# Kernel tuning notes

Measured on AMD Instinct MI355X. Metric: run time of the kernel, lower is better.

## Reference

```python
import jax, jax.numpy as jnp
import numpy as np

N, E, IN_CH, HID, EDGE_DIM, L, G = 50000, 800000, 64, 128, 16, 3, 256

def _bn(h, g, b):
    # BatchNorm1d in training mode (biased batch variance), eps=1e-5
    m = h.mean(0)
    v = ((h - m) ** 2).mean(0)
    return (h - m) * jax.lax.rsqrt(v + 1e-5) * g + b

def setup_inputs() -> dict:
    key = jax.random.key(0)
    ks = jax.random.split(key, 24)
    s = 0.05
    inp = {
        'x': jax.random.normal(ks[0], (N, IN_CH), jnp.float32),
        'edge_attr': jax.random.uniform(ks[1], (E, EDGE_DIM), jnp.float32),
        'src': jax.random.randint(ks[2], (E,), 0, N, jnp.int32),
        'dst': jax.random.randint(ks[3], (E,), 0, N, jnp.int32),
        'batch': jnp.sort(jax.random.randint(ks[4], (N,), 0, G, jnp.int32)),
        'Wp': jax.random.normal(ks[5], (IN_CH, HID), jnp.float32) * s,
        'bp': jnp.zeros((HID,), jnp.float32),
        'conv_We': jax.random.normal(ks[6], (L, EDGE_DIM, HID), jnp.float32) * s,
        'conv_be': jnp.zeros((L, HID), jnp.float32),
        'conv_W1': jax.random.normal(ks[7], (L, HID, HID), jnp.float32) * s,
        'conv_b1': jnp.zeros((L, HID), jnp.float32),
        'conv_g1': jnp.ones((L, HID), jnp.float32),
        'conv_bt1': jnp.zeros((L, HID), jnp.float32),
        'conv_W2': jax.random.normal(ks[8], (L, HID, HID), jnp.float32) * s,
        'conv_b2': jnp.zeros((L, HID), jnp.float32),
        'bn_g': jnp.ones((L, HID), jnp.float32),
        'bn_b': jnp.zeros((L, HID), jnp.float32),
        'head_W1': jax.random.normal(ks[9], (HID * L * 2, HID), jnp.float32) * s,
        'head_b1': jnp.zeros((HID,), jnp.float32),
        'head_g': jnp.ones((HID,), jnp.float32),
        'head_bt': jnp.zeros((HID,), jnp.float32),
        'head_W2': jax.random.normal(ks[10], (HID, 1), jnp.float32) * s,
        'head_b2': jnp.zeros((1,), jnp.float32),
    }
    return inp

def reference(x, edge_attr, src, dst, batch, Wp, bp, conv_We, conv_be, conv_W1, conv_b1,
              conv_g1, conv_bt1, conv_W2, conv_b2, bn_g, bn_b, head_W1, head_b1,
              head_g, head_bt, head_W2, head_b2):
    n = x.shape[0]
    h = x @ Wp + bp  # [N, HID]
    outs = []
    for l in range(L):
        # GINEConv: msg = ReLU(x_src + lin(edge_attr)); sum-aggregate to dst; (1+eps)*x + agg, eps=0
        ee = edge_attr @ conv_We[l] + conv_be[l]          # [E, HID]
        msg = jax.nn.relu(h[src] + ee)                     # [E, HID]
        agg = jax.ops.segment_sum(msg, dst, num_segments=n)
        t = h + agg
        t = t @ conv_W1[l] + conv_b1[l]
        t = jax.nn.relu(_bn(t, conv_g1[l], conv_bt1[l]))
        t = t @ conv_W2[l] + conv_b2[l]
        h = jax.nn.relu(_bn(t, bn_g[l], bn_b[l]))          # outer BN + ReLU (dropout = identity, eval)
        outs.append(h)
    xj = jnp.concatenate(outs, axis=-1)                    # JK 'cat' -> [N, 3*HID]
    cnt = jax.ops.segment_sum(jnp.ones((n,), xj.dtype), batch, num_segments=G)
    z_mean = jax.ops.segment_sum(xj, batch, num_segments=G) / jnp.clip(cnt, 1.0)[:, None]
    z_max = jax.ops.segment_max(xj, batch, num_segments=G)
    z = jnp.concatenate([z_mean, z_max], axis=-1)          # [G, 6*HID]
    z = z @ head_W1 + head_b1
    z = jax.nn.relu(_bn(z, head_g, head_bt))
    return (z @ head_W2 + head_b2).squeeze(-1)             # [G]
```

## Files before the change

kernel.cpp:

```cpp
#include <hip/hip_runtime.h>
#include <hip/hip_bf16.h>

#define HID 128
#define EDIM 16

typedef float v4f __attribute__((ext_vector_type(4)));
typedef float v2f __attribute__((ext_vector_type(2)));
typedef short s8v __attribute__((ext_vector_type(8)));
typedef float f4v __attribute__((ext_vector_type(4)));

#define MFMA_BF16(a, b, c) __builtin_amdgcn_mfma_f32_16x16x32_bf16((a), (b), (c), 0, 0, 0)

__device__ __forceinline__ unsigned short bf16_rne(float v)
{
    unsigned u = __builtin_bit_cast(unsigned, v);
    return (unsigned short)((u + 0x7fffu + ((u >> 16) & 1u)) >> 16);
}

__device__ __forceinline__ void split_bf16(float v, unsigned short& h, unsigned short& l)
{
    unsigned u = __builtin_bit_cast(unsigned, v);
    unsigned hu = (u + 0x7fffu + ((u >> 16) & 1u)) >> 16;
    h = (unsigned short)hu;
    float hf = __builtin_bit_cast(float, hu << 16);
    l = bf16_rne(v - hf);
}

__device__ __forceinline__ v2f vmax0(v2f a)
{
    v2f r; r.x = fmaxf(a.x, 0.f); r.y = fmaxf(a.y, 0.f); return r;
}

__global__ void hist_kernel(const int* __restrict__ dst, int* __restrict__ deg, int E)
{
    int e = blockIdx.x * 256 + threadIdx.x;
    if (e < E) atomicAdd(&deg[dst[e]], 1);
}

__global__ void block_sum_kernel(const int* __restrict__ deg, int* __restrict__ bsum, int Nn)
{
    int i = blockIdx.x * 256 + threadIdx.x;
    int v = (i < Nn) ? deg[i] : 0;
#pragma unroll
    for (int off = 32; off > 0; off >>= 1) v += __shfl_down(v, off, 64);
    __shared__ int ws[4];
    if ((threadIdx.x & 63) == 0) ws[threadIdx.x >> 6] = v;
    __syncthreads();
    if (threadIdx.x == 0) bsum[blockIdx.x] = ws[0] + ws[1] + ws[2] + ws[3];
}

__global__ void bsum_scan_kernel(int* bsum, int nb, int* total_out)
{
    __shared__ int sh[256];
    int tid = threadIdx.x;
    int v = (tid < nb) ? bsum[tid] : 0;
    sh[tid] = v;
    __syncthreads();
    for (int off = 1; off < 256; off <<= 1) {
        int tv = (tid >= off) ? sh[tid - off] : 0;
        __syncthreads();
        sh[tid] += tv;
        __syncthreads();
    }
    if (tid < nb) bsum[tid] = sh[tid] - v;
    if (tid == 255) *total_out = sh[255];
}

__global__ void block_scan_kernel(const int* __restrict__ deg, const int* __restrict__ bsum,
                                  int* __restrict__ row_start, int* __restrict__ cursor, int Nn)
{
    __shared__ int sh[256];
    int tid = threadIdx.x;
    int i = blockIdx.x * 256 + tid;
    int v = (i < Nn) ? deg[i] : 0;
    sh[tid] = v;
    __syncthreads();
    for (int off = 1; off < 256; off <<= 1) {
        int tv = (tid >= off) ? sh[tid - off] : 0;
        __syncthreads();
        sh[tid] += tv;
        __syncthreads();
    }
    if (i < Nn) {
        int excl = sh[tid] - v + bsum[blockIdx.x];
        row_start[i] = excl;
        cursor[i] = excl;
    }
}

template<bool COPY_EA>
__global__ void scatter_kernel(const int* __restrict__ src, const int* __restrict__ dst,
                               int* cursor, int* __restrict__ perm,
                               int* __restrict__ src_perm,
                               const float* __restrict__ ea, float* __restrict__ ea_perm,
                               int E)
{
    int e = blockIdx.x * 256 + threadIdx.x;
    if (e >= E) return;
    int pos = atomicAdd(&cursor[dst[e]], 1);
    src_perm[pos] = src[e];
    if (COPY_EA) {
        const float4* s4 = (const float4*)(ea + (size_t)e * EDIM);
        float4* d4 = (float4*)(ea_perm + (size_t)pos * EDIM);
        d4[0] = s4[0]; d4[1] = s4[1]; d4[2] = s4[2]; d4[3] = s4[3];
    } else {
        perm[pos] = e;
    }
}

__global__ void prep_weights(const float* __restrict__ Wp, const float* __restrict__ W1,
                             const float* __restrict__ W2, unsigned short* __restrict__ out)
{
    int idx = blockIdx.x * 256 + threadIdx.x;
    if (idx < 8192) {
        int n = idx >> 6, k = idx & 63;
        unsigned short h, l;
        split_bf16(Wp[k * 128 + n], h, l);
        out[idx] = h;
        out[8192 + idx] = l;
    } else {
        int j = idx - 8192;
        if (j >= 6 * 16384) return;
        int m2 = j >> 14;
        int r = j & 16383;
        int n = r >> 7, k = r & 127;
        int l = m2 >> 1;
        const float* Wsrc = (m2 & 1) ? (W2 + l * 16384) : (W1 + l * 16384);
        unsigned short h, lo;
        split_bf16(Wsrc[k * 128 + n], h, lo);
        int base = 16384 + m2 * 32768;
        out[base + r] = h;
        out[base + 16384 + r] = lo;
    }
}

__device__ __forceinline__ void matvp(const v4f& a0, const v4f& a1,
                                      const v4f& a2, const v4f& a3,
                                      const v2f* __restrict__ w, v2f& m)
{
    m += w[0] * a0.x;  m += w[1] * a0.y;  m += w[2] * a0.z;  m += w[3] * a0.w;
    m += w[4] * a1.x;  m += w[5] * a1.y;  m += w[6] * a1.z;  m += w[7] * a1.w;
    m += w[8] * a2.x;  m += w[9] * a2.y;  m += w[10] * a2.z; m += w[11] * a2.w;
    m += w[12] * a3.x; m += w[13] * a3.y; m += w[14] * a3.z; m += w[15] * a3.w;
}

template<bool GATH>
__global__ __launch_bounds__(256, 6) void aggregate_kernel(
    const float* __restrict__ h, const float* __restrict__ eaG,
    const int* __restrict__ perm, const int* __restrict__ src_perm,
    const int* __restrict__ row_start,
    const float* __restrict__ We, const float* __restrict__ be,
    float* __restrict__ t, int Nn)
{
    int tid = threadIdx.x;
    int c = (tid & 63) * 2;
    v2f w[16];
#pragma unroll
    for (int k = 0; k < 16; ++k) w[k] = *(const v2f*)&We[k * HID + c];
    v2f bj = *(const v2f*)&be[c];
    int node = blockIdx.x * 4 + (tid >> 6);
    if (node >= Nn) return;
    const float* __restrict__ hc = h + c;
    v2f acc = *(const v2f*)(hc + ((unsigned)node << 7));
    int p0 = __builtin_amdgcn_readfirstlane(row_start[node]);
    int p1 = __builtin_amdgcn_readfirstlane(row_start[node + 1]);
    int p = p0;
    int s0 = 0, s1 = 0, s2 = 0, s3 = 0;
    if (p + 4 <= p1) { s0 = src_perm[p]; s1 = src_perm[p + 1]; s2 = src_perm[p + 2]; s3 = src_perm[p + 3]; }
    while (p + 4 <= p1) {
        int np = p + 4;
        int t0 = 0, t1 = 0, t2 = 0, t3 = 0;
        if (np + 4 <= p1) { t0 = src_perm[np]; t1 = src_perm[np + 1]; t2 = src_perm[np + 2]; t3 = src_perm[np + 3]; }
        v2f h0 = *(const v2f*)(hc + ((unsigned)s0 << 7));
        v2f h1 = *(const v2f*)(hc + ((unsigned)s1 << 7));
        v2f h2 = *(const v2f*)(hc + ((unsigned)s2 << 7));
        v2f h3 = *(const v2f*)(hc + ((unsigned)s3 << 7));
        int q0, q1, q2, q3;
        if (GATH) { q0 = p; q1 = p + 1; q2 = p + 2; q3 = p + 3; }
        else      { q0 = perm[p]; q1 = perm[p + 1]; q2 = perm[p + 2]; q3 = perm[p + 3]; }
        const v4f* e0 = (const v4f*)(eaG + (size_t)(unsigned)q0 * EDIM);
        const v4f* e1 = (const v4f*)(eaG + (size_t)(unsigned)q1 * EDIM);
        const v4f* e2 = (const v4f*)(eaG + (size_t)(unsigned)q2 * EDIM);
        const v4f* e3 = (const v4f*)(eaG + (size_t)(unsigned)q3 * EDIM);
        v4f a00 = e0[0], a01 = e0[1], a02 = e0[2], a03 = e0[3];
        v4f a10 = e1[0], a11 = e1[1], a12 = e1[2], a13 = e1[3];
        v4f a20 = e2[0], a21 = e2[1], a22 = e2[2], a23 = e2[3];
        v4f a30 = e3[0], a31 = e3[1], a32 = e3[2], a33 = e3[3];
        v2f m0 = bj + h0, m1 = bj + h1, m2 = bj + h2, m3 = bj + h3;
        matvp(a00, a01, a02, a03, w, m0);
        matvp(a10, a11, a12, a13, w, m1);
        matvp(a20, a21, a22, a23, w, m2);
        matvp(a30, a31, a32, a33, w, m3);
        acc += vmax0(m0) + vmax0(m1) + vmax0(m2) + vmax0(m3);
        p = np;
        s0 = t0; s1 = t1; s2 = t2; s3 = t3;
    }
    for (; p < p1; ++p) {
        int s = src_perm[p];
        int q = GATH ? p : perm[p];
        const v4f* e0 = (const v4f*)(eaG + (size_t)(unsigned)q * EDIM);
        v4f a0 = e0[0], a1 = e0[1], a2 = e0[2], a3 = e0[3];
        v2f hv = *(const v2f*)(hc + ((unsigned)s << 7));
        v2f m0 = bj + hv;
        matvp(a0, a1, a2, a3, w, m0);
        acc += vmax0(m0);
    }
    *(v2f*)(t + ((unsigned)node << 7) + c) = acc;
}

#define LPAD 40

template<int K, bool PRE_BN, bool POST_STATS>
__global__ __launch_bounds__(256) void gemm_mfma(
    const float* __restrict__ A, const unsigned short* __restrict__ Wh,
    const unsigned short* __restrict__ Wl, const float* __restrict__ bias,
    const float* __restrict__ preStats, const float* __restrict__ preG, const float* __restrict__ preB,
    float* __restrict__ C, float* __restrict__ postStats, int Nrows, float invN)
{
    __shared__ __align__(16) unsigned short Ah[128 * LPAD], Al[128 * LPAD];
    __shared__ __align__(16) unsigned short Bh[128 * LPAD], Bl[128 * LPAD];
    __shared__ float sc[PRE_BN ? K : 1], sb[PRE_BN ? K : 1];
    int tid = threadIdx.x;
    int rbase = blockIdx.x * 128;
    if (PRE_BN) {
        if (tid < K) {
            float mean = preStats[tid] * invN;
            float var = preStats[K + tid] * invN - mean * mean;
            float rstd = rsqrtf(var + 1e-5f);
            float g = preG[tid];
            sc[tid] = rstd * g;
            sb[tid] = preB[tid] - mean * rstd * g;
        }
        __syncthreads();
    }
    int w = tid >> 6, nl = tid & 15, q = (tid >> 4) & 3;
    f4v acc[2][8];
#pragma unroll
    for (int mt = 0; mt < 2; ++mt)
#pragma unroll
        for (int nt = 0; nt < 8; ++nt)
#pragma unroll
            for (int r = 0; r < 4; ++r) acc[mt][nt][r] = 0.f;

    for (int ks = 0; ks < K / 32; ++ks) {
        int k0 = ks * 32;
        if (ks) __syncthreads();
#pragma unroll
        for (int i = 0; i < 4; ++i) {
            int cidx = tid + i * 256;
            int m = cidx >> 3, k4 = (cidx & 7) * 4;
            int gr = rbase + m;
            float4 v = make_float4(0.f, 0.f, 0.f, 0.f);
            if (gr < Nrows) v = *(const float4*)&A[(size_t)gr * K + k0 + k4];
            if (PRE_BN) {
                v.x = fmaxf(v.x * sc[k0 + k4]     + sb[k0 + k4],     0.f);
                v.y = fmaxf(v.y * sc[k0 + k4 + 1] + sb[k0 + k4 + 1], 0.f);
                v.z = fmaxf(v.z * sc[k0 + k4 + 2] + sb[k0 + k4 + 2], 0.f);
                v.w = fmaxf(v.w * sc[k0 + k4 + 3] + sb[k0 + k4 + 3], 0.f);
            }
            unsigned short h0, l0, h1, l1, h2, l2, h3, l3;
            split_bf16(v.x, h0, l0); split_bf16(v.y, h1, l1);
            split_bf16(v.z, h2, l2); split_bf16(v.w, h3, l3);
            uint2 hp, lp;
            hp.x = (unsigned)h0 | ((unsigned)h1 << 16); hp.y = (unsigned)h2 | ((unsigned)h3 << 16);
            lp.x = (unsigned)l0 | ((unsigned)l1 << 16); lp.y = (unsigned)l2 | ((unsigned)l3 << 16);
            *(uint2*)&Ah[m * LPAD + k4] = hp;
            *(uint2*)&Al[m * LPAD + k4] = lp;
        }
#pragma unroll
        for (int i = 0; i < 2; ++i) {
            int g = tid + i * 256;
            int n = g >> 2, kq = (g & 3) * 8;
            uint4 hv = *(const uint4*)&Wh[(size_t)n * K + k0 + kq];
            uint4 lv = *(const uint4*)&Wl[(size_t)n * K + k0 + kq];
            *(uint4*)&Bh[n * LPAD + kq] = hv;
            *(uint4*)&Bl[n * LPAD + kq] = lv;
        }
        __syncthreads();
        s8v ah0 = *(const s8v*)&Ah[(w * 32 + nl) * LPAD + q * 8];
        s8v ah1 = *(const s8v*)&Ah[(w * 32 + 16 + nl) * LPAD + q * 8];
        s8v al0 = *(const s8v*)&Al[(w * 32 + nl) * LPAD + q * 8];
        s8v al1 = *(const s8v*)&Al[(w * 32 + 16 + nl) * LPAD + q * 8];
#pragma unroll
        for (int nt = 0; nt < 8; ++nt) {
            s8v bh = *(const s8v*)&Bh[(nt * 16 + nl) * LPAD + q * 8];
            s8v bl = *(const s8v*)&Bl[(nt * 16 + nl) * LPAD + q * 8];
            acc[0][nt] = MFMA_BF16(ah0, bh, acc[0][nt]);
            acc[0][nt] = MFMA_BF16(ah0, bl, acc[0][nt]);
            acc[0][nt] = MFMA_BF16(al0, bh, acc[0][nt]);
            acc[1][nt] = MFMA_BF16(ah1, bh, acc[1][nt]);
            acc[1][nt] = MFMA_BF16(ah1, bl, acc[1][nt]);
            acc[1][nt] = MFMA_BF16(al1, bh, acc[1][nt]);
        }
    }
    __syncthreads();

    float* redS = (float*)Ah;
    float* redQ = (float*)Al;
#pragma unroll
    for (int nt = 0; nt < 8; ++nt) {
        int col = nt * 16 + nl;
        float bcol = bias[col];
        float sv = 0.f, qv = 0.f;
#pragma unroll
        for (int mt = 0; mt < 2; ++mt) {
#pragma unroll
            for (int r = 0; r < 4; ++r) {
                int grow = rbase + w * 32 + mt * 16 + q * 4 + r;
                if (grow < Nrows) {
                    float o = acc[mt][nt][r] + bcol;
                    C[(size_t)grow * HID + col] = o;
                    if (POST_STATS) { sv += o; qv += o * o; }
                }
            }
        }
        if (POST_STATS) {
            sv += __shfl_down(sv, 32, 64); sv += __shfl_down(sv, 16, 64);
            qv += __shfl_down(qv, 32, 64); qv += __shfl_down(qv, 16, 64);
            if ((tid & 63) < 16) { redS[w * 128 + col] = sv; redQ[w * 128 + col] = qv; }
        }
    }
    if (POST_STATS) {
        __syncthreads();
        if (tid < 128) {
            float S = redS[tid] + redS[128 + tid] + redS[256 + tid] + redS[384 + tid];
            float Q = redQ[tid] + redQ[128 + tid] + redQ[256 + tid] + redQ[384 + tid];
            atomicAdd(&postStats[tid], S);
            atomicAdd(&postStats[128 + tid], Q);
        }
    }
}

__global__ void bn_apply_pool(const float* __restrict__ X, float* __restrict__ h,
                              const float* __restrict__ stats, const float* __restrict__ g,
                              const float* __restrict__ b, const int* __restrict__ starts,
                              float* __restrict__ z, int l, float invN)
{
    int gph = blockIdx.x;
    int tid = threadIdx.x;
    int ch4 = (tid & 31) * 4, wk = tid >> 5;
    float sc[4], sh[4];
#pragma unroll
    for (int u = 0; u < 4; ++u) {
        int j = ch4 + u;
        float mean = stats[j] * invN;
        float var = stats[128 + j] * invN - mean * mean;
        float rstd = rsqrtf(var + 1e-5f);
        float gg = g[j];
        sc[u] = rstd * gg;
        sh[u] = b[j] - mean * rstd * gg;
    }
    int s = starts[gph], e = starts[gph + 1];
    float4 sum = make_float4(0.f, 0.f, 0.f, 0.f);
    float4 mx = make_float4(0.f, 0.f, 0.f, 0.f);
    for (int n = s + wk; n < e; n += 16) {
        float4 v = *(const float4*)&X[(size_t)n * HID + ch4];
        v.x = fmaxf(v.x * sc[0] + sh[0], 0.f);
        v.y = fmaxf(v.y * sc[1] + sh[1], 0.f);
        v.z = fmaxf(v.z * sc[2] + sh[2], 0.f);
        v.w = fmaxf(v.w * sc[3] + sh[3], 0.f);
        *(float4*)&h[(size_t)n * HID + ch4] = v;
        sum.x += v.x; sum.y += v.y; sum.z += v.z; sum.w += v.w;
        mx.x = fmaxf(mx.x, v.x); mx.y = fmaxf(mx.y, v.y);
        mx.z = fmaxf(mx.z, v.z); mx.w = fmaxf(mx.w, v.w);
    }
    __shared__ float ls[16 * 128], lm[16 * 128];
    *(float4*)&ls[wk * 128 + ch4] = sum;
    *(float4*)&lm[wk * 128 + ch4] = mx;
    __syncthreads();
    if (tid < 128) {
        float S = 0.f, M = 0.f;
#pragma unroll
        for (int k = 0; k < 16; ++k) {
            S += ls[k * 128 + tid];
            M = fmaxf(M, lm[k * 128 + tid]);
        }
        float cnt = (float)(e - s);
        z[(size_t)gph * 768 + l * 128 + tid] = S / fmaxf(cnt, 1.f);
        z[(size_t)gph * 768 + 384 + l * 128 + tid] = M;
    }
}

__global__ void starts_kernel(const int* __restrict__ batch, int* __restrict__ starts,
                              int Nn, int Gn)
{
    int g = blockIdx.x * blockDim.x + threadIdx.x;
    if (g > Gn) return;
    int lo = 0, hi = Nn;
    while (lo < hi) { int mid = (lo + hi) >> 1; if (batch[mid] < g) lo = mid + 1; else hi = mid; }
    starts[g] = lo;
}

__global__ void head_gemm1(const float* __restrict__ z, const float* __restrict__ W,
                           const float* __restrict__ bias, float* __restrict__ zr,
                           float* __restrict__ msums)
{
    __shared__ __align__(16) float zl[768];
    int g = blockIdx.x, j = threadIdx.x;
    for (int i = j; i < 768; i += 128) zl[i] = z[(size_t)g * 768 + i];
    __syncthreads();
    float acc = bias[j];
    for (int k = 0; k < 768; k += 4) {
        float4 a4 = *(const float4*)&zl[k];
        acc += a4.x * W[k * 128 + j] + a4.y * W[(k + 1) * 128 + j]
             + a4.z * W[(k + 2) * 128 + j] + a4.w * W[(k + 3) * 128 + j];
    }
    zr[(size_t)g * 128 + j] = acc;
    atomicAdd(&msums[j], acc);
    atomicAdd(&msums[128 + j], acc * acc);
}

__global__ void head_final(const float* __restrict__ zr, const float* __restrict__ msums,
                           const float* __restrict__ hg, const float* __restrict__ hb,
                           const float* __restrict__ W2, const float* __restrict__ b2,
                           float* __restrict__ out, float invG)
{
    int g = blockIdx.x, j = threadIdx.x;
    float mean = msums[j] * invG;
    float var = msums[128 + j] * invG - mean * mean;
    float rstd = rsqrtf(var + 1e-5f);
    float v = zr[(size_t)g * 128 + j];
    v = (v - mean) * rstd * hg[j] + hb[j];
    v = fmaxf(v, 0.f);
    float p = v * W2[j];
#pragma unroll
    for (int off = 32; off > 0; off >>= 1) p += __shfl_down(p, off, 64);
    __shared__ float partial[2];
    if ((j & 63) == 0) partial[j >> 6] = p;
    __syncthreads();
    if (j == 0) out[g] = partial[0] + partial[1] + b2[0];
}

extern "C" void kernel_launch(void* const* d_in, const int* in_sizes, int n_in,
                              void* d_out, int out_size, void* d_ws, size_t ws_size,
                              hipStream_t stream)
{
    const float* x         = (const float*)d_in[0];
    const float* edge_attr = (const float*)d_in[1];
    const int*   src       = (const int*)d_in[2];
    const int*   dst       = (const int*)d_in[3];
    const int*   batch     = (const int*)d_in[4];
    const float* Wp        = (const float*)d_in[5];
    const float* bp        = (const float*)d_in[6];
    const float* conv_We   = (const float*)d_in[7];
    const float* conv_be   = (const float*)d_in[8];
    const float* conv_W1   = (const float*)d_in[9];
    const float* conv_b1   = (const float*)d_in[10];
    const float* conv_g1   = (const float*)d_in[11];
    const float* conv_bt1  = (const float*)d_in[12];
    const float* conv_W2   = (const float*)d_in[13];
    const float* conv_b2   = (const float*)d_in[14];
    const float* bn_g      = (const float*)d_in[15];
    const float* bn_b      = (const float*)d_in[16];
    const float* head_W1   = (const float*)d_in[17];
    const float* head_b1   = (const float*)d_in[18];
    const float* head_g    = (const float*)d_in[19];
    const float* head_bt   = (const float*)d_in[20];
    const float* head_W2   = (const float*)d_in[21];
    const float* head_b2   = (const float*)d_in[22];

    const int N = in_sizes[4];
    const int E = in_sizes[2];
    const int G = out_size;
    const int L = 3;

    float* h        = (float*)d_ws;
    float* t        = h + (size_t)N * HID;
    float* z        = t + (size_t)N * HID;
    float* zr       = z + (size_t)G * 768;
    float* statsAll = zr + (size_t)G * HID;
    int*   deg      = (int*)(statsAll + 7 * 256);
    int*   starts   = deg + N;
    int*   row_start= starts + (G + 1);
    int*   cursor   = row_start + (N + 1);
    int*   bsum     = cursor + N;
    int*   src_perm = bsum + 256;
    int*   perm     = src_perm + E;
    unsigned short* wt = (unsigned short*)(perm + E);
    size_t base_end = (size_t)((char*)(wt + 212992) - (char*)d_ws);
    size_t ea_off = (base_end + 15) & ~(size_t)15;
    bool gath = (ea_off + (size_t)E * EDIM * sizeof(float)) <= ws_size;
    float* ea_perm = (float*)((char*)d_ws + ea_off);
    float* msums = statsAll + 6 * 256;

    (void)n_in;

    const float invN = 1.0f / (float)N;
    const float invG = 1.0f / (float)G;
    const int nb = (N + 255) / 256;
    const int gemmBlocks = (N + 127) / 128;

    (void)hipMemsetAsync(statsAll, 0, 7 * 256 * sizeof(float) + (size_t)N * sizeof(int), stream);
    hist_kernel<<<(E + 255) / 256, 256, 0, stream>>>(dst, deg, E);
    block_sum_kernel<<<nb, 256, 0, stream>>>(deg, bsum, N);
    bsum_scan_kernel<<<1, 256, 0, stream>>>(bsum, nb, &row_start[N]);
    block_scan_kernel<<<nb, 256, 0, stream>>>(deg, bsum, row_start, cursor, N);
    if (gath)
        scatter_kernel<true><<<(E + 255) / 256, 256, 0, stream>>>(
            src, dst, cursor, perm, src_perm, edge_attr, ea_perm, E);
    else
        scatter_kernel<false><<<(E + 255) / 256, 256, 0, stream>>>(
            src, dst, cursor, perm, src_perm, edge_attr, ea_perm, E);
    starts_kernel<<<1, 512, 0, stream>>>(batch, starts, N, G);
    prep_weights<<<(8192 + 6 * 16384 + 255) / 256, 256, 0, stream>>>(Wp, conv_W1, conv_W2, wt);

    const unsigned short* Wp_hi = wt;
    const unsigned short* Wp_lo = wt + 8192;

    gemm_mfma<64, false, false><<<gemmBlocks, 256, 0, stream>>>(
        x, Wp_hi, Wp_lo, bp, nullptr, nullptr, nullptr, h, nullptr, N, invN);

    for (int l = 0; l < L; ++l) {
        float* sI = statsAll + l * 512;
        float* sO = sI + 256;
        const unsigned short* W1hi = wt + 16384 + (size_t)(2 * l) * 32768;
        const unsigned short* W1lo = W1hi + 16384;
        const unsigned short* W2hi = wt + 16384 + (size_t)(2 * l + 1) * 32768;
        const unsigned short* W2lo = W2hi + 16384;
        if (gath)
            aggregate_kernel<true><<<(N + 3) / 4, 256, 0, stream>>>(
                h, ea_perm, perm, src_perm, row_start,
                conv_We + (size_t)l * EDIM * HID, conv_be + l * HID, t, N);
        else
            aggregate_kernel<false><<<(N + 3) / 4, 256, 0, stream>>>(
                h, edge_attr, perm, src_perm, row_start,
                conv_We + (size_t)l * EDIM * HID, conv_be + l * HID, t, N);
        gemm_mfma<128, false, true><<<gemmBlocks, 256, 0, stream>>>(
            t, W1hi, W1lo, conv_b1 + l * HID,
            nullptr, nullptr, nullptr, t, sI, N, invN);
        gemm_mfma<128, true, true><<<gemmBlocks, 256, 0, stream>>>(
            t, W2hi, W2lo, conv_b2 + l * HID,
            sI, conv_g1 + l * HID, conv_bt1 + l * HID, t, sO, N, invN);
        bn_apply_pool<<<G, 512, 0, stream>>>(
            t, h, sO, bn_g + l * HID, bn_b + l * HID, starts, z, l, invN);
    }

    head_gemm1<<<G, 128, 0, stream>>>(z, head_W1, head_b1, zr, msums);
    head_final<<<G, 128, 0, stream>>>(zr, msums, head_g, head_bt, head_W2, head_b2,
                                      (float*)d_out, invG);
}
```

Measured before the change: 719.2 us.

## Store node features and permuted edge attributes as bf16 to halve gather traffic

Node features h and the dst-sorted edge attributes are now stored in bf16 instead of fp32. The projection GEMM and the BN/pool kernel write packed bf16, and the aggregation kernel unpacks these values on load. This targets the memory-bound gathers in aggregation and also raises the occupancy hint. Non-temporal stores are used in the scatter kernel. The cost is reduced precision on h and edge_attr, which may affect accuracy against the fp32 reference.

```diff
diff --git a/kernel.cpp b/kernel.cpp
--- a/kernel.cpp
+++ b/kernel.cpp
@@ -6,6 +6,7 @@
 
 typedef float v4f __attribute__((ext_vector_type(4)));
 typedef float v2f __attribute__((ext_vector_type(2)));
+typedef unsigned v4u __attribute__((ext_vector_type(4)));
 typedef short s8v __attribute__((ext_vector_type(8)));
 typedef float f4v __attribute__((ext_vector_type(4)));
 
@@ -15,6 +16,24 @@
 {
     unsigned u = __builtin_bit_cast(unsigned, v);
     return (unsigned short)((u + 0x7fffu + ((u >> 16) & 1u)) >> 16);
+}
+
+__device__ __forceinline__ unsigned pack2(float lo, float hi)
+{
+    return (unsigned)bf16_rne(lo) | ((unsigned)bf16_rne(hi) << 16);
+}
+
+__device__ __forceinline__ float bflo(unsigned u) { return __builtin_bit_cast(float, u << 16); }
+__device__ __forceinline__ float bfhi(unsigned u) { return __builtin_bit_cast(float, u & 0xffff0000u); }
+
+__device__ __forceinline__ v2f unpack2(unsigned u)
+{
+    v2f r; r.x = bflo(u); r.y = bfhi(u); return r;
+}
+
+__device__ __forceinline__ v4f unpack4(unsigned a, unsigned b)
+{
+    v4f r; r.x = bflo(a); r.y = bfhi(a); r.z = bflo(b); r.w = bfhi(b); return r;
 }
 
 __device__ __forceinline__ void split_bf16(float v, unsigned short& h, unsigned short& l)
@@ -92,17 +111,24 @@
 __global__ void scatter_kernel(const int* __restrict__ src, const int* __restrict__ dst,
                                int* cursor, int* __restrict__ perm,
                                int* __restrict__ src_perm,
-                               const float* __restrict__ ea, float* __restrict__ ea_perm,
+                               const float* __restrict__ ea, unsigned short* __restrict__ ea16,
                                int E)
 {
     int e = blockIdx.x * 256 + threadIdx.x;
     if (e >= E) return;
     int pos = atomicAdd(&cursor[dst[e]], 1);
-    src_perm[pos] = src[e];
+    __builtin_nontemporal_store(src[e], &src_perm[pos]);
     if (COPY_EA) {
         const float4* s4 = (const float4*)(ea + (size_t)e * EDIM);
-        float4* d4 = (float4*)(ea_perm + (size_t)pos * EDIM);
-        d4[0] = s4[0]; d4[1] = s4[1]; d4[2] = s4[2]; d4[3] = s4[3];
+        float4 a = s4[0], b = s4[1], c = s4[2], d = s4[3];
+        v4u u0, u1;
+        u0.x = pack2(a.x, a.y); u0.y = pack2(a.z, a.w);
+        u0.z = pack2(b.x, b.y); u0.w = pack2(b.z, b.w);
+        u1.x = pack2(c.x, c.y); u1.y = pack2(c.z, c.w);
+        u1.z = pack2(d.x, d.y); u1.w = pack2(d.z, d.w);
+        v4u* dp = (v4u*)(ea16 + (size_t)pos * EDIM);
+        __builtin_nontemporal_store(u0, dp);
+        __builtin_nontemporal_store(u1, dp + 1);
     } else {
         perm[pos] = e;
     }
@@ -145,63 +171,86 @@
 }
 
 template<bool GATH>
-__global__ __launch_bounds__(256, 6) void aggregate_kernel(
-    const float* __restrict__ h, const float* __restrict__ eaG,
+__global__ __launch_bounds__(256, 8) void aggregate_kernel(
+    const unsigned short* __restrict__ h16, const unsigned short* __restrict__ ea16,
+    const float* __restrict__ eaf,
     const int* __restrict__ perm, const int* __restrict__ src_perm,
     const int* __restrict__ row_start,
     const float* __restrict__ We, const float* __restrict__ be,
     float* __restrict__ t, int Nn)
 {
     int tid = threadIdx.x;
-    int c = (tid & 63) * 2;
+    int lane = tid & 63;
+    int c = lane * 2;
     v2f w[16];
 #pragma unroll
     for (int k = 0; k < 16; ++k) w[k] = *(const v2f*)&We[k * HID + c];
     v2f bj = *(const v2f*)&be[c];
     int node = blockIdx.x * 4 + (tid >> 6);
     if (node >= Nn) return;
-    const float* __restrict__ hc = h + c;
-    v2f acc = *(const v2f*)(hc + ((unsigned)node << 7));
+    const unsigned* __restrict__ hw = (const unsigned*)h16 + lane;
+    v2f acc = unpack2(hw[(unsigned)node << 6]);
     int p0 = __builtin_amdgcn_readfirstlane(row_start[node]);
     int p1 = __builtin_amdgcn_readfirstlane(row_start[node + 1]);
     int p = p0;
+    const unsigned* ep = (const unsigned*)ea16 + (size_t)(unsigned)p0 * 8u;
     int s0 = 0, s1 = 0, s2 = 0, s3 = 0;
     if (p + 4 <= p1) { s0 = src_perm[p]; s1 = src_perm[p + 1]; s2 = src_perm[p + 2]; s3 = src_perm[p + 3]; }
     while (p + 4 <= p1) {
         int np = p + 4;
         int t0 = 0, t1 = 0, t2 = 0, t3 = 0;
         if (np + 4 <= p1) { t0 = src_perm[np]; t1 = src_perm[np + 1]; t2 = src_perm[np + 2]; t3 = src_perm[np + 3]; }
-        v2f h0 = *(const v2f*)(hc + ((unsigned)s0 << 7));
-        v2f h1 = *(const v2f*)(hc + ((unsigned)s1 << 7));
-        v2f h2 = *(const v2f*)(hc + ((unsigned)s2 << 7));
-        v2f h3 = *(const v2f*)(hc + ((unsigned)s3 << 7));
-        int q0, q1, q2, q3;
-        if (GATH) { q0 = p; q1 = p + 1; q2 = p + 2; q3 = p + 3; }
-        else      { q0 = perm[p]; q1 = perm[p + 1]; q2 = perm[p + 2]; q3 = perm[p + 3]; }
-        const v4f* e0 = (const v4f*)(eaG + (size_t)(unsigned)q0 * EDIM);
-        const v4f* e1 = (const v4f*)(eaG + (size_t)(unsigned)q1 * EDIM);
-        const v4f* e2 = (const v4f*)(eaG + (size_t)(unsigned)q2 * EDIM);
-        const v4f* e3 = (const v4f*)(eaG + (size_t)(unsigned)q3 * EDIM);
-        v4f a00 = e0[0], a01 = e0[1], a02 = e0[2], a03 = e0[3];
-        v4f a10 = e1[0], a11 = e1[1], a12 = e1[2], a13 = e1[3];
-        v4f a20 = e2[0], a21 = e2[1], a22 = e2[2], a23 = e2[3];
-        v4f a30 = e3[0], a31 = e3[1], a32 = e3[2], a33 = e3[3];
-        v2f m0 = bj + h0, m1 = bj + h1, m2 = bj + h2, m3 = bj + h3;
+        unsigned hu0 = hw[(unsigned)s0 << 6];
+        unsigned hu1 = hw[(unsigned)s1 << 6];
+        unsigned hu2 = hw[(unsigned)s2 << 6];
+        unsigned hu3 = hw[(unsigned)s3 << 6];
+        v4f a00, a01, a02, a03, a10, a11, a12, a13;
+        v4f a20, a21, a22, a23, a30, a31, a32, a33;
+        if (GATH) {
+            unsigned ua[32];
+#pragma unroll
+            for (int i = 0; i < 32; ++i) ua[i] = ep[i];
+            a00 = unpack4(ua[0], ua[1]);   a01 = unpack4(ua[2], ua[3]);
+            a02 = unpack4(ua[4], ua[5]);   a03 = unpack4(ua[6], ua[7]);
+            a10 = unpack4(ua[8], ua[9]);   a11 = unpack4(ua[10], ua[11]);
+            a12 = unpack4(ua[12], ua[13]); a13 = unpack4(ua[14], ua[15]);
+            a20 = unpack4(ua[16], ua[17]); a21 = unpack4(ua[18], ua[19]);
+            a22 = unpack4(ua[20], ua[21]); a23 = unpack4(ua[22], ua[23]);
+            a30 = unpack4(ua[24], ua[25]); a31 = unpack4(ua[26], ua[27]);
+            a32 = unpack4(ua[28], ua[29]); a33 = unpack4(ua[30], ua[31]);
+        } else {
+            const v4f* e0 = (const v4f*)(eaf + (size_t)(unsigned)perm[p] * EDIM);
+            const v4f* e1 = (const v4f*)(eaf + (size_t)(unsigned)perm[p + 1] * EDIM);
+            const v4f* e2 = (const v4f*)(eaf + (size_t)(unsigned)perm[p + 2] * EDIM);
+            const v4f* e3 = (const v4f*)(eaf + (size_t)(unsigned)perm[p + 3] * EDIM);
+            a00 = e0[0]; a01 = e0[1]; a02 = e0[2]; a03 = e0[3];
+            a10 = e1[0]; a11 = e1[1]; a12 = e1[2]; a13 = e1[3];
+            a20 = e2[0]; a21 = e2[1]; a22 = e2[2]; a23 = e2[3];
+            a30 = e3[0]; a31 = e3[1]; a32 = e3[2]; a33 = e3[3];
+        }
+        v2f m0 = bj + unpack2(hu0), m1 = bj + unpack2(hu1);
+        v2f m2 = bj + unpack2(hu2), m3 = bj + unpack2(hu3);
         matvp(a00, a01, a02, a03, w, m0);
         matvp(a10, a11, a12, a13, w, m1);
         matvp(a20, a21, a22, a23, w, m2);
         matvp(a30, a31, a32, a33, w, m3);
         acc += vmax0(m0) + vmax0(m1) + vmax0(m2) + vmax0(m3);
+        ep += 32;
         p = np;
         s0 = t0; s1 = t1; s2 = t2; s3 = t3;
     }
     for (; p < p1; ++p) {
         int s = src_perm[p];
-        int q = GATH ? p : perm[p];
-        const v4f* e0 = (const v4f*)(eaG + (size_t)(unsigned)q * EDIM);
-        v4f a0 = e0[0], a1 = e0[1], a2 = e0[2], a3 = e0[3];
-        v2f hv = *(const v2f*)(hc + ((unsigned)s << 7));
-        v2f m0 = bj + hv;
+        v4f a0, a1, a2, a3;
+        if (GATH) {
+            const unsigned* er = (const unsigned*)ea16 + (size_t)(unsigned)p * 8u;
+            a0 = unpack4(er[0], er[1]); a1 = unpack4(er[2], er[3]);
+            a2 = unpack4(er[4], er[5]); a3 = unpack4(er[6], er[7]);
+        } else {
+            const v4f* e0 = (const v4f*)(eaf + (size_t)(unsigned)perm[p] * EDIM);
+            a0 = e0[0]; a1 = e0[1]; a2 = e0[2]; a3 = e0[3];
+        }
+        v2f m0 = bj + unpack2(hw[(unsigned)s << 6]);
         matvp(a0, a1, a2, a3, w, m0);
         acc += vmax0(m0);
     }
@@ -210,12 +259,12 @@
 
 #define LPAD 40
 
-template<int K, bool PRE_BN, bool POST_STATS>
+template<int K, bool PRE_BN, bool POST_STATS, bool OUT_BF16>
 __global__ __launch_bounds__(256) void gemm_mfma(
     const float* __restrict__ A, const unsigned short* __restrict__ Wh,
     const unsigned short* __restrict__ Wl, const float* __restrict__ bias,
     const float* __restrict__ preStats, const float* __restrict__ preG, const float* __restrict__ preB,
-    float* __restrict__ C, float* __restrict__ postStats, int Nrows, float invN)
+    void* __restrict__ Cout, float* __restrict__ postStats, int Nrows, float invN)
 {
     __shared__ __align__(16) unsigned short Ah[128 * LPAD], Al[128 * LPAD];
     __shared__ __align__(16) unsigned short Bh[128 * LPAD], Bl[128 * LPAD];
@@ -295,6 +344,8 @@
     }
     __syncthreads();
 
+    float* Cf = (float*)Cout;
+    unsigned short* Ch = (unsigned short*)Cout;
     float* redS = (float*)Ah;
     float* redQ = (float*)Al;
 #pragma unroll
@@ -309,7 +360,8 @@
                 int grow = rbase + w * 32 + mt * 16 + q * 4 + r;
                 if (grow < Nrows) {
                     float o = acc[mt][nt][r] + bcol;
-                    C[(size_t)grow * HID + col] = o;
+                    if (OUT_BF16) Ch[(size_t)grow * HID + col] = bf16_rne(o);
+                    else          Cf[(size_t)grow * HID + col] = o;
                     if (POST_STATS) { sv += o; qv += o * o; }
                 }
             }
@@ -331,7 +383,7 @@
     }
 }
 
-__global__ void bn_apply_pool(const float* __restrict__ X, float* __restrict__ h,
+__global__ void bn_apply_pool(const float* __restrict__ X, unsigned short* __restrict__ h16,
                               const float* __restrict__ stats, const float* __restrict__ g,
                               const float* __restrict__ b, const int* __restrict__ starts,
                               float* __restrict__ z, int l, float invN)
@@ -353,13 +405,17 @@
     int s = starts[gph], e = starts[gph + 1];
     float4 sum = make_float4(0.f, 0.f, 0.f, 0.f);
     float4 mx = make_float4(0.f, 0.f, 0.f, 0.f);
+    unsigned* hv32 = (unsigned*)h16;
     for (int n = s + wk; n < e; n += 16) {
         float4 v = *(const float4*)&X[(size_t)n * HID + ch4];
         v.x = fmaxf(v.x * sc[0] + sh[0], 0.f);
         v.y = fmaxf(v.y * sc[1] + sh[1], 0.f);
         v.z = fmaxf(v.z * sc[2] + sh[2], 0.f);
         v.w = fmaxf(v.w * sc[3] + sh[3], 0.f);
-        *(float4*)&h[(size_t)n * HID + ch4] = v;
+        uint2 pk;
+        pk.x = pack2(v.x, v.y);
+        pk.y = pack2(v.z, v.w);
+        *(uint2*)&hv32[(size_t)n * 64 + (ch4 >> 1)] = pk;
         sum.x += v.x; sum.y += v.y; sum.z += v.z; sum.w += v.w;
         mx.x = fmaxf(mx.x, v.x); mx.y = fmaxf(mx.y, v.y);
         mx.z = fmaxf(mx.z, v.z); mx.w = fmaxf(mx.w, v.w);
@@ -464,9 +520,9 @@
     const int G = out_size;
     const int L = 3;
 
-    float* h        = (float*)d_ws;
-    float* t        = h + (size_t)N * HID;
-    float* z        = t + (size_t)N * HID;
+    float* t        = (float*)d_ws;
+    unsigned short* h16 = (unsigned short*)(t + (size_t)N * HID);
+    float* z        = (float*)(h16 + (size_t)N * HID);
     float* zr       = z + (size_t)G * 768;
     float* statsAll = zr + (size_t)G * HID;
     int*   deg      = (int*)(statsAll + 7 * 256);
@@ -479,8 +535,8 @@
     unsigned short* wt = (unsigned short*)(perm + E);
     size_t base_end = (size_t)((char*)(wt + 212992) - (char*)d_ws);
     size_t ea_off = (base_end + 15) & ~(size_t)15;
-    bool gath = (ea_off + (size_t)E * EDIM * sizeof(float)) <= ws_size;
-    float* ea_perm = (float*)((char*)d_ws + ea_off);
+    bool gath = (ea_off + (size_t)E * EDIM * sizeof(unsigned short)) <= ws_size;
+    unsigned short* ea16 = (unsigned short*)((char*)d_ws + ea_off);
     float* msums = statsAll + 6 * 256;
 
     (void)n_in;
@@ -497,18 +553,18 @@
     block_scan_kernel<<<nb, 256, 0, stream>>>(deg, bsum, row_start, cursor, N);
     if (gath)
         scatter_kernel<true><<<(E + 255) / 256, 256, 0, stream>>>(
-            src, dst, cursor, perm, src_perm, edge_attr, ea_perm, E);
+            src, dst, cursor, perm, src_perm, edge_attr, ea16, E);
     else
         scatter_kernel<false><<<(E + 255) / 256, 256, 0, stream>>>(
-            src, dst, cursor, perm, src_perm, edge_attr, ea_perm, E);
+            src, dst, cursor, perm, src_perm, edge_attr, ea16, E);
     starts_kernel<<<1, 512, 0, stream>>>(batch, starts, N, G);
     prep_weights<<<(8192 + 6 * 16384 + 255) / 256, 256, 0, stream>>>(Wp, conv_W1, conv_W2, wt);
 
     const unsigned short* Wp_hi = wt;
     const unsigned short* Wp_lo = wt + 8192;
 
-    gemm_mfma<64, false, false><<<gemmBlocks, 256, 0, stream>>>(
-        x, Wp_hi, Wp_lo, bp, nullptr, nullptr, nullptr, h, nullptr, N, invN);
+    gemm_mfma<64, false, false, true><<<gemmBlocks, 256, 0, stream>>>(
+        x, Wp_hi, Wp_lo, bp, nullptr, nullptr, nullptr, h16, nullptr, N, invN);
 
     for (int l = 0; l < L; ++l) {
         float* sI = statsAll + l * 512;
@@ -519,20 +575,20 @@
         const unsigned short* W2lo = W2hi + 16384;
         if (gath)
             aggregate_kernel<true><<<(N + 3) / 4, 256, 0, stream>>>(
-                h, ea_perm, perm, src_perm, row_start,
+                h16, ea16, edge_attr, perm, src_perm, row_start,
                 conv_We + (size_t)l * EDIM * HID, conv_be + l * HID, t, N);
         else
             aggregate_kernel<false><<<(N + 3) / 4, 256, 0, stream>>>(
-                h, edge_attr, perm, src_perm, row_start,
+                h16, ea16, edge_attr, perm, src_perm, row_start,
                 conv_We + (size_t)l * EDIM * HID, conv_be + l * HID, t, N);
-        gemm_mfma<128, false, true><<<gemmBlocks, 256, 0, stream>>>(
+        gemm_mfma<128, false, true, false><<<gemmBlocks, 256, 0, stream>>>(
             t, W1hi, W1lo, conv_b1 + l * HID,
             nullptr, nullptr, nullptr, t, sI, N, invN);
-        gemm_mfma<128, true, true><<<gemmBlocks, 256, 0, stream>>>(
+        gemm_mfma<128, true, true, false><<<gemmBlocks, 256, 0, stream>>>(
             t, W2hi, W2lo, conv_b2 + l * HID,
             sI, conv_g1 + l * HID, conv_bt1 + l * HID, t, sO, N, invN);
         bn_apply_pool<<<G, 512, 0, stream>>>(
-            t, h, sO, bn_g + l * HID, bn_b + l * HID, starts, z, l, invN);
+            t, h16, sO, bn_g + l * HID, bn_b + l * HID, starts, z, l, invN);
     }
 
     head_gemm1<<<G, 128, 0, stream>>>(z, head_W1, head_b1, zr, msums);
```

Measured after the change: 788.4 us. 1.1x slower.
